# Kernel optimization log

Measured on AMD Instinct MI355X. Metric: run time of the kernel, lower is better.

The kernel has to match this reference:

```python
import jax, jax.numpy as jnp
import numpy as np

B, N, C = 2, 9216, 512
HEAD, SR = 8, 4
R = 32  # lora rank
SCALING = 4.0 / 32.0  # alpha / r


def setup_inputs() -> dict:
    key = jax.random.key(0)
    ks = jax.random.split(key, 16)
    s = 0.02
    inp = {
        "x": jax.random.normal(ks[0], (B, N, C), jnp.float32),
        "w_q": jax.random.normal(ks[1], (C, C), jnp.float32) * s,
        "b_q": jnp.zeros((C,), jnp.float32),
        "w_kv": jax.random.normal(ks[2], (2 * C, C), jnp.float32) * s,
        "b_kv": jnp.zeros((2 * C,), jnp.float32),
        "w_proj": jax.random.normal(ks[3], (C, C), jnp.float32) * s,
        "b_proj": jnp.zeros((C,), jnp.float32),
        "w_sr": jax.random.normal(ks[4], (C, C, SR, SR), jnp.float32) * s,
        "b_sr": jnp.zeros((C,), jnp.float32),
        "ln_g": jnp.ones((C,), jnp.float32),
        "ln_b": jnp.zeros((C,), jnp.float32),
        "lora_A_q": jax.random.normal(ks[5], (R, C), jnp.float32) * s,
        "lora_B_q": jax.random.normal(ks[6], (C, R), jnp.float32) * s,
        "lora_A_v": jax.random.normal(ks[7], (R, C), jnp.float32) * s,
        "lora_B_v": jax.random.normal(ks[8], (C, R), jnp.float32) * s,
        "H": 96,
        "W": 96,
    }
    return inp


def reference(x, w_q, b_q, w_kv, b_kv, w_proj, b_proj, w_sr, b_sr,
              ln_g, ln_b, lora_A_q, lora_B_q, lora_A_v, lora_B_v, H, W):
    b, n, c = x.shape
    d = c // HEAD
    # q = Linear(x) + LoRA(x) * scaling
    q = x @ w_q.T + b_q + ((x @ lora_A_q.T) @ lora_B_q.T) * SCALING
    q = q.reshape(b, n, HEAD, d).transpose(0, 2, 1, 3)  # (B, h, N, d)
    # spatial reduction: Conv2d(dim, dim, sr, sr) then LayerNorm
    xi = x.transpose(0, 2, 1).reshape(b, c, H, W)
    xs = jax.lax.conv_general_dilated(
        xi, w_sr, window_strides=(SR, SR), padding='VALID',
        dimension_numbers=('NCHW', 'OIHW', 'NCHW'))
    xs = xs + b_sr[None, :, None, None]
    xs = xs.reshape(b, c, -1).transpose(0, 2, 1)  # (B, Nkv, C)
    mu = jnp.mean(xs, axis=-1, keepdims=True)
    var = jnp.var(xs, axis=-1, keepdims=True)
    xs = (xs - mu) * jax.lax.rsqrt(var + 1e-5) * ln_g + ln_b
    # k, v
    kv = (xs @ w_kv.T + b_kv).reshape(b, -1, 2, HEAD, d).transpose(2, 0, 3, 1, 4)
    k, v = kv[0], kv[1]  # (B, h, Nkv, d)
    lv = ((xs @ lora_A_v.T) @ lora_B_v.T) * SCALING  # (B, Nkv, C)
    # faithful to torch: raw memory reshape, NOT a head-transpose
    v = v + lv.reshape(b, HEAD, -1, d)
    # attention
    attn = jax.nn.softmax(jnp.einsum('bhnd,bhmd->bhnm', q, k) * (d ** -0.5), axis=-1)
    out = jnp.einsum('bhnm,bhmd->bhnd', attn, v).transpose(0, 2, 1, 3).reshape(b, n, c)
    return out @ w_proj.T + b_proj
```

## Files before the change

### kernel.cpp

```cpp
#include <hip/hip_runtime.h>

typedef __attribute__((ext_vector_type(8))) __bf16 bf16x8;
typedef __attribute__((ext_vector_type(4))) float f32x4;
typedef __attribute__((ext_vector_type(4))) unsigned int u32x4;

#define MFMA16(a, b, c) __builtin_amdgcn_mfma_f32_16x16x32_bf16((a), (b), (c), 0, 0, 0)

__device__ __forceinline__ bool input_is_f32(const void* ln_g) {
    return ((const unsigned*)ln_g)[0] == 0x3F800000u;
}

__device__ __forceinline__ float rdf(const void* p, long i, bool f32) {
    return f32 ? ((const float*)p)[i] : (float)((const __bf16*)p)[i];
}

__device__ __forceinline__ void conv_big(const void* s, __bf16* d, long base, bool f) {
    long i = base + (long)threadIdx.x * 8;
    if (f) {
        f32x4 a = ((const f32x4*)s)[i / 4];
        f32x4 b = ((const f32x4*)s)[i / 4 + 1];
        bf16x8 o;
        #pragma unroll
        for (int j = 0; j < 4; ++j) { o[j] = (__bf16)a[j]; o[4 + j] = (__bf16)b[j]; }
        *(bf16x8*)(d + i) = o;
    } else {
        *(u32x4*)(d + i) = ((const u32x4*)s)[i / 8];
    }
}

__device__ __forceinline__ void conv_small(const void* s, __bf16* d, int n, bool f) {
    int i = threadIdx.x * 4;
    if (i < n) {
        #pragma unroll
        for (int j = 0; j < 4; ++j)
            d[i + j] = f ? (__bf16)((const float*)s)[i + j] : ((const __bf16*)s)[i + j];
    }
}

__global__ void convert_kernel(const void* x, const void* w_kv, const void* w_proj,
                               const void* b_q, const void* b_kv, const void* b_proj,
                               const void* b_sr, const void* ln_g, const void* ln_b,
                               __bf16* x_b, __bf16* w_kv_b, __bf16* w_proj_b,
                               __bf16* b_q_b, __bf16* b_kv_b, __bf16* b_proj_b,
                               __bf16* b_sr_b, __bf16* ln_g_b, __bf16* ln_b_b) {
    const bool f = input_is_f32(ln_g);
    int blk = blockIdx.x;
    if (blk < 4608)      conv_big(x, x_b, (long)blk * 2048, f);
    else if (blk < 4864) conv_big(w_kv, w_kv_b, (long)(blk - 4608) * 2048, f);
    else if (blk < 4992) conv_big(w_proj, w_proj_b, (long)(blk - 4864) * 2048, f);
    else if (blk == 4992) conv_small(b_q, b_q_b, 512, f);
    else if (blk == 4993) conv_small(b_kv, b_kv_b, 1024, f);
    else if (blk == 4994) conv_small(b_proj, b_proj_b, 512, f);
    else if (blk == 4995) conv_small(b_sr, b_sr_b, 512, f);
    else if (blk == 4996) conv_small(ln_g, ln_g_b, 512, f);
    else                  conv_small(ln_b, ln_b_b, 512, f);
}

__global__ void prep_kernel(const void* __restrict__ w_q,
                            const void* __restrict__ Aq, const void* __restrict__ Bq,
                            const void* __restrict__ Av, const void* __restrict__ Bv,
                            const void* __restrict__ w_sr, const void* __restrict__ ln_g,
                            __bf16* __restrict__ w_q_eff, __bf16* __restrict__ w_lv,
                            __bf16* __restrict__ w_sr_t) {
    const bool f = input_is_f32(ln_g);
    int tid = blockIdx.x * 256 + threadIdx.x;
    if (tid < 262144) {
        int o = tid >> 9, c = tid & 511;
        float acc = 0.f;
        #pragma unroll 8
        for (int r = 0; r < 32; ++r)
            acc += rdf(Bq, o * 32 + r, f) * rdf(Aq, r * 512 + c, f);
        w_q_eff[tid] = (__bf16)(rdf(w_q, tid, f) + 0.125f * acc);
    } else if (tid < 524288) {
        int t = tid - 262144;
        int o = t >> 9, c = t & 511;
        float acc = 0.f;
        #pragma unroll 8
        for (int r = 0; r < 32; ++r)
            acc += rdf(Bv, o * 32 + r, f) * rdf(Av, r * 512 + c, f);
        w_lv[t] = (__bf16)(0.125f * acc);
    } else if (tid < 786432) {
        int t = tid - 524288;
        int o = t >> 9, i = t & 511;
        #pragma unroll
        for (int p = 0; p < 16; ++p)
            w_sr_t[(size_t)o * 8192 + p * 512 + i] = (__bf16)rdf(w_sr, (long)t * 16 + p, f);
    }
}

__global__ __launch_bounds__(256) void gemm128(const __bf16* __restrict__ A,
                                               const __bf16* __restrict__ Bt,
                                               const __bf16* __restrict__ bias,
                                               void* __restrict__ out, int mode) {
    __shared__ __attribute__((aligned(16))) char lds[16384];
    char* As = lds;
    char* Bs = lds + 8192;
    const int tid = threadIdx.x;
    const int m0 = blockIdx.x << 7, n0 = blockIdx.y << 7;
    const int w = tid >> 6, lane = tid & 63;
    const int wm = (w >> 1) << 6, wn = (w & 1) << 6;
    const int lr = lane & 15, lg = lane >> 4;

    f32x4 acc[4][4] = {};

    const int srow = tid >> 1;
    const int sc0 = (tid & 1) * 2;
    const __bf16* Arow = A + (size_t)(m0 + srow) * 512;
    const __bf16* Brow = Bt + (size_t)(n0 + srow) * 512;

    for (int k0 = 0; k0 < 512; k0 += 32) {
        u32x4 a0 = *(const u32x4*)(Arow + k0 + sc0 * 8);
        u32x4 a1 = *(const u32x4*)(Arow + k0 + sc0 * 8 + 8);
        u32x4 b0 = *(const u32x4*)(Brow + k0 + sc0 * 8);
        u32x4 b1 = *(const u32x4*)(Brow + k0 + sc0 * 8 + 8);
        __syncthreads();
        *(u32x4*)(As + srow * 64 + sc0 * 16) = a0;
        *(u32x4*)(As + srow * 64 + sc0 * 16 + 16) = a1;
        *(u32x4*)(Bs + srow * 64 + sc0 * 16) = b0;
        *(u32x4*)(Bs + srow * 64 + sc0 * 16 + 16) = b1;
        __syncthreads();
        bf16x8 a[4], b[4];
        #pragma unroll
        for (int i = 0; i < 4; ++i)
            a[i] = *(const bf16x8*)(As + (wm + i * 16 + lr) * 64 + lg * 16);
        #pragma unroll
        for (int j = 0; j < 4; ++j)
            b[j] = *(const bf16x8*)(Bs + (wn + j * 16 + lr) * 64 + lg * 16);
        #pragma unroll
        for (int i = 0; i < 4; ++i)
            #pragma unroll
            for (int j = 0; j < 4; ++j)
                acc[i][j] = MFMA16(a[i], b[j], acc[i][j]);
    }

    #pragma unroll
    for (int j = 0; j < 4; ++j) {
        int col = n0 + wn + j * 16 + lr;
        float bv = (float)bias[col];
        #pragma unroll
        for (int i = 0; i < 4; ++i) {
            int rb = m0 + wm + i * 16 + lg * 4;
            #pragma unroll
            for (int r = 0; r < 4; ++r) {
                float v = acc[i][j][r] + bv;
                int grow = rb + r;
                if (mode == 0) {
                    ((float*)out)[(size_t)grow * 512 + col] = v;
                } else {
                    int b_ = grow >= 9216 ? 1 : 0;
                    int nn = grow - b_ * 9216;
                    ((__bf16*)out)[(((size_t)(b_ * 8 + (col >> 6))) * 9216 + nn) * 64 +
                                   (col & 63)] = (__bf16)v;
                }
            }
        }
    }
}

__global__ __launch_bounds__(256) void conv_gemm(const __bf16* __restrict__ x,
                                                 const __bf16* __restrict__ Wt,
                                                 float* __restrict__ part) {
    __shared__ __attribute__((aligned(16))) char lds[18432];
    char* As = lds;
    char* Bs = lds + 9216;
    const int tid = threadIdx.x;
    const int m0 = blockIdx.x << 6, n0 = blockIdx.y << 6;
    const int kz = blockIdx.z;
    const int kbase = kz << 10;
    const int w = tid >> 6, lane = tid & 63;
    const int wm = (w >> 1) << 5, wn = (w & 1) << 5;
    const int lr = lane & 15, lg = lane >> 4;

    const int srow = tid >> 2, sc = tid & 3;
    int m = m0 + srow;
    int bb = m >= 576 ? 1 : 0;
    int rem = m - bb * 576;
    int oy = rem / 24;
    int ox = rem - oy * 24;
    const __bf16* xrow = x + ((size_t)bb * 9216 + oy * 384 + ox * 4) * 512;
    const __bf16* brow = Wt + (size_t)(n0 + srow) * 8192;

    f32x4 acc[2][2] = {};
    for (int kk = 0; kk < 1024; kk += 64) {
        int k0 = kbase + kk;
        int p = k0 >> 9;
        int i0 = k0 & 511;
        int ky = p >> 2, kx = p & 3;
        const __bf16* xsrc = xrow + ((ky * 96 + kx) << 9) + i0;
        __syncthreads();
        #pragma unroll
        for (int j = 0; j < 2; ++j) {
            int c = sc + j * 4;
            u32x4 av = *(const u32x4*)(xsrc + c * 8);
            u32x4 bv = *(const u32x4*)(brow + k0 + c * 8);
            *(u32x4*)(As + srow * 144 + c * 16) = av;
            *(u32x4*)(Bs + srow * 144 + c * 16) = bv;
        }
        __syncthreads();
        bf16x8 a[2][2], b[2][2];
        #pragma unroll
        for (int i = 0; i < 2; ++i)
            #pragma unroll
            for (int ks = 0; ks < 2; ++ks) {
                a[i][ks] = *(const bf16x8*)(As + (wm + i * 16 + lr) * 144 + ks * 64 + lg * 16);
                b[i][ks] = *(const bf16x8*)(Bs + (wn + i * 16 + lr) * 144 + ks * 64 + lg * 16);
            }
        #pragma unroll
        for (int i = 0; i < 2; ++i)
            #pragma unroll
            for (int j = 0; j < 2; ++j)
                #pragma unroll
                for (int ks = 0; ks < 2; ++ks)
                    acc[i][j] = MFMA16(a[i][ks], b[j][ks], acc[i][j]);
    }
    float* pout = part + (size_t)kz * 589824;
    #pragma unroll
    for (int j = 0; j < 2; ++j) {
        int col = n0 + wn + j * 16 + lr;
        #pragma unroll
        for (int i = 0; i < 2; ++i) {
            int rb = m0 + wm + i * 16 + lg * 4;
            #pragma unroll
            for (int r = 0; r < 4; ++r)
                pout[(size_t)(rb + r) * 512 + col] = acc[i][j][r];
        }
    }
}

__global__ __launch_bounds__(64) void lnorm(const float* __restrict__ parts,
                                            const __bf16* __restrict__ b_sr,
                                            const __bf16* __restrict__ g,
                                            const __bf16* __restrict__ be,
                                            __bf16* __restrict__ out) {
    int row = blockIdx.x;
    int lane = threadIdx.x;
    const float* xr = parts + (size_t)row * 512;
    float v[8], s = 0.f, sq = 0.f;
    #pragma unroll
    for (int i = 0; i < 8; ++i) {
        int c = lane + i * 64;
        float t = (float)b_sr[c];
        #pragma unroll
        for (int sp = 0; sp < 8; ++sp)
            t += xr[(size_t)sp * 589824 + c];
        v[i] = t;
        s += t;
        sq += t * t;
    }
    #pragma unroll
    for (int d = 1; d < 64; d <<= 1) {
        s += __shfl_xor(s, d);
        sq += __shfl_xor(sq, d);
    }
    float mean = s * (1.0f / 512.0f);
    float var = sq * (1.0f / 512.0f) - mean * mean;
    float rstd = rsqrtf(var + 1e-5f);
    __bf16* orow = out + (size_t)row * 512;
    #pragma unroll
    for (int i = 0; i < 8; ++i) {
        int c = lane + i * 64;
        orow[c] = (__bf16)((v[i] - mean) * rstd * (float)g[c] + (float)be[c]);
    }
}

__global__ __launch_bounds__(256) void kv_gemm(const __bf16* __restrict__ xs,
                                               const __bf16* __restrict__ w_kv,
                                               const __bf16* __restrict__ w_lv,
                                               const __bf16* __restrict__ b_kv,
                                               __bf16* __restrict__ k_t,
                                               float* __restrict__ v_raw,
                                               __bf16* __restrict__ lv) {
    __shared__ __attribute__((aligned(16))) char lds[18432];
    char* As = lds;
    char* Bs = lds + 9216;
    const int tid = threadIdx.x;
    const int m0 = blockIdx.x << 6, n0 = blockIdx.y << 6;
    const int w = tid >> 6, lane = tid & 63;
    const int wm = (w >> 1) << 5, wn = (w & 1) << 5;
    const int lr = lane & 15, lg = lane >> 4;

    const int srow = tid >> 2, sc = tid & 3;
    const __bf16* arow = xs + (size_t)(m0 + srow) * 512;
    const __bf16* brow = (n0 < 1024) ? (w_kv + (size_t)(n0 + srow) * 512)
                                     : (w_lv + (size_t)(n0 - 1024 + srow) * 512);

    f32x4 acc[2][2] = {};
    for (int k0 = 0; k0 < 512; k0 += 64) {
        __syncthreads();
        #pragma unroll
        for (int j = 0; j < 2; ++j) {
            int c = sc + j * 4;
            u32x4 av = *(const u32x4*)(arow + k0 + c * 8);
            u32x4 bv = *(const u32x4*)(brow + k0 + c * 8);
            *(u32x4*)(As + srow * 144 + c * 16) = av;
            *(u32x4*)(Bs + srow * 144 + c * 16) = bv;
        }
        __syncthreads();
        bf16x8 a[2][2], b[2][2];
        #pragma unroll
        for (int i = 0; i < 2; ++i)
            #pragma unroll
            for (int ks = 0; ks < 2; ++ks) {
                a[i][ks] = *(const bf16x8*)(As + (wm + i * 16 + lr) * 144 + ks * 64 + lg * 16);
                b[i][ks] = *(const bf16x8*)(Bs + (wn + i * 16 + lr) * 144 + ks * 64 + lg * 16);
            }
        #pragma unroll
        for (int i = 0; i < 2; ++i)
            #pragma unroll
            for (int j = 0; j < 2; ++j)
                #pragma unroll
                for (int ks = 0; ks < 2; ++ks)
                    acc[i][j] = MFMA16(a[i][ks], b[j][ks], acc[i][j]);
    }
    #pragma unroll
    for (int j = 0; j < 2; ++j) {
        int col = n0 + wn + j * 16 + lr;
        float bv = (col < 1024) ? (float)b_kv[col] : 0.0f;
        #pragma unroll
        for (int i = 0; i < 2; ++i) {
            int rb = m0 + wm + i * 16 + lg * 4;
            #pragma unroll
            for (int r = 0; r < 4; ++r) {
                int grow = rb + r;
                float val = acc[i][j][r] + bv;
                int b_ = grow >= 576 ? 1 : 0;
                int mm = grow - b_ * 576;
                if (col < 512) {
                    int h = col >> 6, dd = col & 63;
                    k_t[(((size_t)(b_ * 8 + h)) * 576 + mm) * 64 + dd] = (__bf16)val;
                } else if (col < 1024) {
                    v_raw[((size_t)b_ * 576 + mm) * 512 + (col - 512)] = val;
                } else {
                    lv[((size_t)b_ * 576 + mm) * 512 + (col - 1024)] = (__bf16)val;
                }
            }
        }
    }
}

__global__ void v_fixup(const float* __restrict__ v_raw, const __bf16* __restrict__ lv,
                        __bf16* __restrict__ vT) {
    int tid = blockIdx.x * 256 + threadIdx.x;
    if (tid >= 589824) return;
    int mm = tid % 576;
    int rest = tid / 576;
    int dd = rest & 63;
    int bh = rest >> 6;
    int b_ = bh >> 3, h = bh & 7;
    int flat = h * 36864 + mm * 64 + dd;
    int n2 = flat >> 9, c2 = flat & 511;
    float val = v_raw[((size_t)b_ * 576 + mm) * 512 + h * 64 + dd] +
                (float)lv[((size_t)b_ * 576 + n2) * 512 + c2];
    vT[tid] = (__bf16)val;
}

__global__ __launch_bounds__(256) void attn_kernel(const __bf16* __restrict__ q_t,
                                                   const __bf16* __restrict__ k_t,
                                                   const __bf16* __restrict__ vT,
                                                   __bf16* __restrict__ attnv) {
    __shared__ __attribute__((aligned(16))) char lds[4608 + 5120 + 10240];
    char* Ks = lds;
    char* Vs = lds + 4608;
    char* Ps = lds + 9728;
    const int tid = threadIdx.x;
    const int w = tid >> 6, lane = tid & 63;
    const int lr = lane & 15, lg = lane >> 4;
    const int bh = blockIdx.y;
    const int qrow0 = (blockIdx.x << 7) + (w << 5);
    char* Psw = Ps + w * 2560;

    bf16x8 qf[2][2];
    #pragma unroll
    for (int mt = 0; mt < 2; ++mt)
        #pragma unroll
        for (int ks = 0; ks < 2; ++ks)
            qf[mt][ks] = *(const bf16x8*)(q_t + ((size_t)bh * 9216 + qrow0 + mt * 16 + lr) * 64 +
                                          ks * 32 + lg * 8);

    f32x4 oacc[2][4] = {};
    float lsum[2][4] = {};

    const int krow = tid >> 3, kc = tid & 7;
    const int vrow = tid >> 2, vc = tid & 3;

    for (int kv0 = 0; kv0 < 576; kv0 += 32) {
        __syncthreads();
        *(u32x4*)(Ks + krow * 144 + kc * 16) =
            *(const u32x4*)(k_t + ((size_t)bh * 576 + kv0 + krow) * 64 + kc * 8);
        *(u32x4*)(Vs + vrow * 80 + vc * 16) =
            *(const u32x4*)(vT + ((size_t)bh * 64 + vrow) * 576 + kv0 + vc * 8);
        __syncthreads();
        bf16x8 kf[2][2];
        #pragma unroll
        for (int nt = 0; nt < 2; ++nt)
            #pragma unroll
            for (int ks = 0; ks < 2; ++ks)
                kf[nt][ks] = *(const bf16x8*)(Ks + (nt * 16 + lr) * 144 + ks * 64 + lg * 16);
        f32x4 s[2][2] = {};
        #pragma unroll
        for (int mt = 0; mt < 2; ++mt)
            #pragma unroll
            for (int nt = 0; nt < 2; ++nt)
                #pragma unroll
                for (int ks = 0; ks < 2; ++ks)
                    s[mt][nt] = MFMA16(qf[mt][ks], kf[nt][ks], s[mt][nt]);
        #pragma unroll
        for (int mt = 0; mt < 2; ++mt)
            #pragma unroll
            for (int nt = 0; nt < 2; ++nt)
                #pragma unroll
                for (int r = 0; r < 4; ++r) {
                    float p = __expf(s[mt][nt][r] * 0.125f);
                    __bf16 pb = (__bf16)p;
                    lsum[mt][r] += (float)pb;
                    *(__bf16*)(Psw + (mt * 16 + lg * 4 + r) * 80 + (nt * 16 + lr) * 2) = pb;
                }
        __syncthreads();
        bf16x8 pf[2], vf[4];
        #pragma unroll
        for (int mt = 0; mt < 2; ++mt)
            pf[mt] = *(const bf16x8*)(Psw + (mt * 16 + lr) * 80 + lg * 16);
        #pragma unroll
        for (int nd = 0; nd < 4; ++nd)
            vf[nd] = *(const bf16x8*)(Vs + (nd * 16 + lr) * 80 + lg * 16);
        #pragma unroll
        for (int mt = 0; mt < 2; ++mt)
            #pragma unroll
            for (int nd = 0; nd < 4; ++nd)
                oacc[mt][nd] = MFMA16(pf[mt], vf[nd], oacc[mt][nd]);
    }

    #pragma unroll
    for (int mt = 0; mt < 2; ++mt)
        #pragma unroll
        for (int r = 0; r < 4; ++r) {
            float t = lsum[mt][r];
            t += __shfl_xor(t, 1);
            t += __shfl_xor(t, 2);
            t += __shfl_xor(t, 4);
            t += __shfl_xor(t, 8);
            lsum[mt][r] = 1.0f / t;
        }
    const int b_ = bh >> 3, h = bh & 7;
    #pragma unroll
    for (int mt = 0; mt < 2; ++mt)
        #pragma unroll
        for (int nd = 0; nd < 4; ++nd)
            #pragma unroll
            for (int r = 0; r < 4; ++r) {
                int row = qrow0 + mt * 16 + lg * 4 + r;
                int col = h * 64 + nd * 16 + lr;
                attnv[((size_t)b_ * 9216 + row) * 512 + col] =
                    (__bf16)(oacc[mt][nd][r] * lsum[mt][r]);
            }
}

extern "C" void kernel_launch(void* const* d_in, const int* in_sizes, int n_in,
                              void* d_out, int out_size, void* d_ws, size_t ws_size,
                              hipStream_t stream) {
    const void* x      = d_in[0];
    const void* w_q    = d_in[1];
    const void* b_q    = d_in[2];
    const void* w_kv   = d_in[3];
    const void* b_kv   = d_in[4];
    const void* w_proj = d_in[5];
    const void* b_proj = d_in[6];
    const void* w_sr   = d_in[7];
    const void* b_sr   = d_in[8];
    const void* ln_g   = d_in[9];
    const void* ln_b   = d_in[10];
    const void* A_q    = d_in[11];
    const void* B_q    = d_in[12];
    const void* A_v    = d_in[13];
    const void* B_v    = d_in[14];

    char* ws = (char*)d_ws;
    __bf16* x_b      = (__bf16*)(ws);
    __bf16* attnv    = (__bf16*)(ws);
    float*  parts    = (float*)(ws + 18874368);
    __bf16* q_t      = (__bf16*)(ws + 18874368);
    __bf16* k_t      = (__bf16*)(ws + 37748736);
    __bf16* vT       = (__bf16*)(ws + 38928384);
    __bf16* w_q_eff  = (__bf16*)(ws + 40108032);
    __bf16* w_lv     = (__bf16*)(ws + 40632320);
    __bf16* w_sr_t   = (__bf16*)(ws + 41156608);
    __bf16* w_kv_b   = (__bf16*)(ws + 49545216);
    __bf16* w_proj_b = (__bf16*)(ws + 50593792);
    __bf16* xs_ln    = (__bf16*)(ws + 53477376);
    float*  v_raw    = (float*)(ws + 54657024);
    __bf16* lv       = (__bf16*)(ws + 57016320);
    __bf16* b_q_b    = (__bf16*)(ws + 58195968);
    __bf16* b_kv_b   = (__bf16*)(ws + 58196992);
    __bf16* b_proj_b = (__bf16*)(ws + 58199040);
    __bf16* b_sr_b   = (__bf16*)(ws + 58200064);
    __bf16* ln_g_b   = (__bf16*)(ws + 58201088);
    __bf16* ln_b_b   = (__bf16*)(ws + 58202112);

    convert_kernel<<<4998, 256, 0, stream>>>(x, w_kv, w_proj, b_q, b_kv, b_proj,
                                             b_sr, ln_g, ln_b,
                                             x_b, w_kv_b, w_proj_b, b_q_b, b_kv_b,
                                             b_proj_b, b_sr_b, ln_g_b, ln_b_b);
    prep_kernel<<<3072, 256, 0, stream>>>(w_q, A_q, B_q, A_v, B_v, w_sr, ln_g,
                                          w_q_eff, w_lv, w_sr_t);
    conv_gemm<<<dim3(18, 8, 8), 256, 0, stream>>>(x_b, w_sr_t, parts);
    lnorm<<<1152, 64, 0, stream>>>(parts, b_sr_b, ln_g_b, ln_b_b, xs_ln);
    gemm128<<<dim3(144, 4), 256, 0, stream>>>(x_b, w_q_eff, b_q_b, q_t, 1);
    kv_gemm<<<dim3(18, 24), 256, 0, stream>>>(xs_ln, w_kv_b, w_lv, b_kv_b, k_t, v_raw, lv);
    v_fixup<<<2304, 256, 0, stream>>>(v_raw, lv, vT);
    attn_kernel<<<dim3(72, 16), 256, 0, stream>>>(q_t, k_t, vT, attnv);
    gemm128<<<dim3(144, 4), 256, 0, stream>>>(attnv, w_proj_b, b_proj_b, d_out, 0);
}
```

Measured before the change: 283.7 us.

## Use direct global-to-LDS loads in GEMM and register-fed K/V in attention

The 128x128 GEMM now stages A and B tiles with global_load_lds DMA instructions, replacing the load-to-register then store-to-LDS round trip. The layout is rearranged so each thread writes one contiguous 16-byte slot. The attention kernel no longer stages K and V tiles in shared memory: each wave reads its MFMA fragments straight from global memory, and all block-wide barriers in the KV loop are removed. Only the per-wave P buffer stays in LDS. The trade-off is that every wave re-reads the same K/V data through the cache instead of sharing it, and correctness relies on in-order LDS access within a wave for the P buffer.

New measurement: 332.6 us. +17.2%, slower.

```diff
diff --git a/kernel.cpp b/kernel.cpp
--- a/kernel.cpp
+++ b/kernel.cpp
@@ -5,6 +5,12 @@
 typedef __attribute__((ext_vector_type(4))) unsigned int u32x4;
 
 #define MFMA16(a, b, c) __builtin_amdgcn_mfma_f32_16x16x32_bf16((a), (b), (c), 0, 0, 0)
+
+__device__ __forceinline__ void gload_lds16(const void* g, void* l) {
+    __builtin_amdgcn_global_load_lds(
+        (__attribute__((address_space(1))) void*)(g),
+        (__attribute__((address_space(3))) void*)(l), 16, 0, 0);
+}
 
 __device__ __forceinline__ bool input_is_f32(const void* ln_g) {
     return ((const unsigned*)ln_g)[0] == 0x3F800000u;
@@ -103,21 +109,18 @@
 
     f32x4 acc[4][4] = {};
 
-    const int srow = tid >> 1;
-    const int sc0 = (tid & 1) * 2;
-    const __bf16* Arow = A + (size_t)(m0 + srow) * 512;
-    const __bf16* Brow = Bt + (size_t)(n0 + srow) * 512;
+    const int soff0 = tid * 16;
+    const int arow0 = tid >> 2;
+    const int akb = (tid & 3) * 8;
+    const __bf16* Abase = A + (size_t)m0 * 512;
+    const __bf16* Bbase = Bt + (size_t)n0 * 512;
 
     for (int k0 = 0; k0 < 512; k0 += 32) {
-        u32x4 a0 = *(const u32x4*)(Arow + k0 + sc0 * 8);
-        u32x4 a1 = *(const u32x4*)(Arow + k0 + sc0 * 8 + 8);
-        u32x4 b0 = *(const u32x4*)(Brow + k0 + sc0 * 8);
-        u32x4 b1 = *(const u32x4*)(Brow + k0 + sc0 * 8 + 8);
         __syncthreads();
-        *(u32x4*)(As + srow * 64 + sc0 * 16) = a0;
-        *(u32x4*)(As + srow * 64 + sc0 * 16 + 16) = a1;
-        *(u32x4*)(Bs + srow * 64 + sc0 * 16) = b0;
-        *(u32x4*)(Bs + srow * 64 + sc0 * 16 + 16) = b1;
+        gload_lds16(Abase + (size_t)arow0 * 512 + k0 + akb, As + soff0);
+        gload_lds16(Abase + (size_t)(arow0 + 64) * 512 + k0 + akb, As + soff0 + 4096);
+        gload_lds16(Bbase + (size_t)arow0 * 512 + k0 + akb, Bs + soff0);
+        gload_lds16(Bbase + (size_t)(arow0 + 64) * 512 + k0 + akb, Bs + soff0 + 4096);
         __syncthreads();
         bf16x8 a[4], b[4];
         #pragma unroll
@@ -358,10 +361,7 @@
                                                    const __bf16* __restrict__ k_t,
                                                    const __bf16* __restrict__ vT,
                                                    __bf16* __restrict__ attnv) {
-    __shared__ __attribute__((aligned(16))) char lds[4608 + 5120 + 10240];
-    char* Ks = lds;
-    char* Vs = lds + 4608;
-    char* Ps = lds + 9728;
+    __shared__ __attribute__((aligned(16))) char Ps[10240];
     const int tid = threadIdx.x;
     const int w = tid >> 6, lane = tid & 63;
     const int lr = lane & 15, lg = lane >> 4;
@@ -369,6 +369,9 @@
     const int qrow0 = (blockIdx.x << 7) + (w << 5);
     char* Psw = Ps + w * 2560;
 
+    const __bf16* kbase = k_t + (size_t)bh * 576 * 64;
+    const __bf16* vbase = vT + (size_t)bh * 64 * 576;
+
     bf16x8 qf[2][2];
     #pragma unroll
     for (int mt = 0; mt < 2; ++mt)
@@ -380,22 +383,18 @@
     f32x4 oacc[2][4] = {};
     float lsum[2][4] = {};
 
-    const int krow = tid >> 3, kc = tid & 7;
-    const int vrow = tid >> 2, vc = tid & 3;
-
     for (int kv0 = 0; kv0 < 576; kv0 += 32) {
-        __syncthreads();
-        *(u32x4*)(Ks + krow * 144 + kc * 16) =
-            *(const u32x4*)(k_t + ((size_t)bh * 576 + kv0 + krow) * 64 + kc * 8);
-        *(u32x4*)(Vs + vrow * 80 + vc * 16) =
-            *(const u32x4*)(vT + ((size_t)bh * 64 + vrow) * 576 + kv0 + vc * 8);
-        __syncthreads();
-        bf16x8 kf[2][2];
+        bf16x8 kf[2][2], vf[4];
         #pragma unroll
         for (int nt = 0; nt < 2; ++nt)
             #pragma unroll
             for (int ks = 0; ks < 2; ++ks)
-                kf[nt][ks] = *(const bf16x8*)(Ks + (nt * 16 + lr) * 144 + ks * 64 + lg * 16);
+                kf[nt][ks] = *(const bf16x8*)(kbase + (size_t)(kv0 + nt * 16 + lr) * 64 +
+                                              ks * 32 + lg * 8);
+        #pragma unroll
+        for (int nd = 0; nd < 4; ++nd)
+            vf[nd] = *(const bf16x8*)(vbase + (size_t)(nd * 16 + lr) * 576 + kv0 + lg * 8);
+
         f32x4 s[2][2] = {};
         #pragma unroll
         for (int mt = 0; mt < 2; ++mt)
@@ -415,14 +414,10 @@
                     lsum[mt][r] += (float)pb;
                     *(__bf16*)(Psw + (mt * 16 + lg * 4 + r) * 80 + (nt * 16 + lr) * 2) = pb;
                 }
-        __syncthreads();
-        bf16x8 pf[2], vf[4];
+        bf16x8 pf[2];
         #pragma unroll
         for (int mt = 0; mt < 2; ++mt)
             pf[mt] = *(const bf16x8*)(Psw + (mt * 16 + lr) * 80 + lg * 16);
-        #pragma unroll
-        for (int nd = 0; nd < 4; ++nd)
-            vf[nd] = *(const bf16x8*)(Vs + (nd * 16 + lr) * 80 + lg * 16);
         #pragma unroll
         for (int mt = 0; mt < 2; ++mt)
             #pragma unroll
```
